# Kernel optimization log

Measured on AMD Instinct MI355X. Metric: run time of the kernel, lower is better.

## Reference

```python
import jax, jax.numpy as jnp
import numpy as np
from itertools import product


def _gen_exps(num_vars, degree):
    return [e for e in product(range(degree + 1), repeat=num_vars) if sum(e) <= degree]

EXPS_W = _gen_exps(4, 3)  # 35 tuples (ex, es, ey, ew)
EXPS_B = _gen_exps(2, 3)  # 10 tuples (ey, eb)


def setup_inputs() -> dict:
    key = jax.random.key(0)
    ks = jax.random.split(key, 7)
    B, D_in, D_out = 8192, 512, 512
    x = jax.random.normal(ks[0], (B, D_in), dtype=jnp.float32)
    s = jax.random.normal(ks[1], (B, D_out), dtype=jnp.float32)
    y = jax.random.normal(ks[2], (B, D_out), dtype=jnp.float32)
    w = jax.random.normal(ks[3], (D_out, D_in), dtype=jnp.float32) * 0.05
    b = jax.random.normal(ks[4], (D_out,), dtype=jnp.float32) * 0.05
    params_w = jax.random.normal(ks[5], (len(EXPS_W),), dtype=jnp.float32) * 0.1
    params_b = jax.random.normal(ks[6], (len(EXPS_B),), dtype=jnp.float32) * 0.1
    return {"x": x, "s": s, "y": y, "w": w, "b": b, "params_w": params_w, "params_b": params_b}


def _dw(x, s, y, w, params_w):
    # unique exponent powers (computed once, reused across the 35 terms)
    px = {e: x ** e for e in {t[0] for t in EXPS_W}}
    ps = {e: s ** e for e in {t[1] for t in EXPS_W}}
    py = {e: y ** e for e in {t[2] for t in EXPS_W}}
    pw = {e: w ** e for e in {t[3] for t in EXPS_W}}
    inv_B = 1.0 / x.shape[0]
    delta_w = jnp.zeros_like(w)
    for i, (ex, es, ey, ew) in enumerate(EXPS_W):
        # (y^ey * s^es).T @ x^ex  -> [out, in]
        corr = jnp.einsum("bo,bi->oi", py[ey] * ps[es], px[ex])
        delta_w = delta_w + (params_w[i] * inv_B) * corr * pw[ew]
    # bound=None -> identity; l2_reg=0.0
    return delta_w


def _db(y, b, params_b):
    py = {e: y ** e for e in {t[0] for t in EXPS_B}}
    pb = {e: b ** e for e in {t[1] for t in EXPS_B}}
    inv_B = 1.0 / y.shape[0]
    delta_b = jnp.zeros_like(b)
    for i, (ey, eb) in enumerate(EXPS_B):
        delta_b = delta_b + (params_b[i] * inv_B) * jnp.sum(py[ey], axis=0) * pb[eb]
    return delta_b


def reference(x, s, y, w, b, params_w, params_b):
    delta_w = _dw(x, s, y, w, params_w)
    delta_b = _db(y, b, params_b)
    return delta_w, delta_b
```

## Files before the change

kernel.cpp:

```cpp
#include <hip/hip_runtime.h>

#define BD 8192
#define DD 512
#define PLANE (BD * DD)
#define NPLANES 5
#define KSPLIT 32
#define NELEM (DD * DD)

typedef __attribute__((ext_vector_type(4))) float f32x4;
typedef __attribute__((ext_vector_type(8))) short short8;

__device__ __forceinline__ float polyev2(float c0, float c1, float c2, float w, float w2) {
    return c0 + c1 * w + c2 * w2;
}

__device__ __forceinline__ unsigned short f2b(float v) {
    unsigned u = __builtin_bit_cast(unsigned, v);
    u += 0x7FFFu + ((u >> 16) & 1u);
    return (unsigned short)(u >> 16);
}

__device__ __forceinline__ void gload_lds16(const unsigned short* g, unsigned short* l) {
    __builtin_amdgcn_global_load_lds((__attribute__((address_space(1))) const void*)g,
                                     (__attribute__((address_space(3))) void*)l, 16, 0, 0);
}


__global__ __launch_bounds__(256, 3) void prep3_kernel(
    const float* __restrict__ x, const float* __restrict__ s,
    const float* __restrict__ y, const float* __restrict__ pw,
    unsigned short* __restrict__ pl, float* __restrict__ csp)
{
    __shared__ char L[5 * 8192];

    const int t      = threadIdx.x;
    const int colL4  = (t & 15) * 4;
    const int rg     = t >> 4;
    const int kl     = rg * 4;
    const int c0     = blockIdx.x * 64;
    const int bt     = blockIdx.y;
    const int r0     = bt * 64;

    const float p23 = pw[23], p24 = pw[24], p25 = pw[25], p26 = pw[26], p27 = pw[27];
    const float p28 = pw[28], p29 = pw[29], p32 = pw[32], p33 = pw[33];

    float sm[12][4];
#pragma unroll
    for (int v = 0; v < 12; ++v)
#pragma unroll
        for (int cc = 0; cc < 4; ++cc) sm[v][cc] = 0.f;

    unsigned pk[NPLANES][4][2];

#pragma unroll
    for (int j = 0; j < 4; ++j) {
        const int row = r0 + kl + j;
        const float4 xv = *(const float4*)&x[(size_t)row * DD + c0 + colL4];
        const float4 sv = *(const float4*)&s[(size_t)row * DD + c0 + colL4];
        const float4 yv = *(const float4*)&y[(size_t)row * DD + c0 + colL4];
        const float xa[4] = {xv.x, xv.y, xv.z, xv.w};
        const float sa[4] = {sv.x, sv.y, sv.z, sv.w};
        const float ya[4] = {yv.x, yv.y, yv.z, yv.w};
#pragma unroll
        for (int cc = 0; cc < 4; ++cc) {
            const float X = xa[cc], S = sa[cc], Y = ya[cc];
            const float X2 = X * X, S2 = S * S, Y2 = Y * Y, SY = S * Y;
            sm[0][cc] += X;  sm[1][cc] += X2;      sm[2][cc] += X2 * X;
            sm[3][cc] += S;  sm[4][cc] += S2;      sm[5][cc] += S2 * S;
            sm[6][cc] += Y;  sm[7][cc] += Y2;      sm[8][cc] += Y2 * Y;
            sm[9][cc] += SY; sm[10][cc] += S2 * Y; sm[11][cc] += S * Y2;
            unsigned short tv[NPLANES];
            tv[0] = f2b(p26 * S + p23 * Y + p29 * S2 + p25 * Y2 + p28 * SY);
            tv[1] = f2b(p33 * S + p32 * Y);
            tv[2] = f2b(p27 * S + p24 * Y);
            tv[3] = f2b(X);
            tv[4] = f2b(X2);
            if ((j & 1) == 0) {
#pragma unroll
                for (int p = 0; p < NPLANES; ++p) pk[p][cc][j >> 1] = (unsigned)tv[p];
            } else {
#pragma unroll
                for (int p = 0; p < NPLANES; ++p) pk[p][cc][j >> 1] |= (unsigned)tv[p] << 16;
            }
        }
    }

#pragma unroll
    for (int p = 0; p < NPLANES; ++p) {
#pragma unroll
        for (int cc = 0; cc < 4; ++cc) {
            const int colL = colL4 + cc;
            const int addr = p * 8192 + colL * 128 + (((kl >> 3) ^ (colL & 7)) << 4) + ((kl & 4) << 1);
            uint2 u; u.x = pk[p][cc][0]; u.y = pk[p][cc][1];
            *(uint2*)&L[addr] = u;
        }
    }
    __syncthreads();

    {
        char* gbase = (char*)pl;
        const size_t blockByte = ((size_t)bt * DD + c0) * 128;
#pragma unroll
        for (int u = 0; u < 10; ++u) {
            const int byteoff = u * 4096 + t * 16;
            const int p = byteoff >> 13;
            const int within = byteoff & 8191;
            *(uint4*)(gbase + ((size_t)p * PLANE) * 2 + blockByte + within) =
                *(const uint4*)&L[byteoff];
        }
    }
    __syncthreads();

#pragma unroll
    for (int v = 0; v < 12; ++v)
#pragma unroll
        for (int cc = 0; cc < 4; ++cc) {
            sm[v][cc] += __shfl_xor(sm[v][cc], 16, 64);
            sm[v][cc] += __shfl_xor(sm[v][cc], 32, 64);
        }
    float* R = (float*)L;
    const int wv = t >> 6, ln = t & 63;
    if (ln < 16) {
#pragma unroll
        for (int v = 0; v < 12; ++v)
#pragma unroll
            for (int cc = 0; cc < 4; ++cc)
                R[(wv * 16 + ln) * 48 + v * 4 + cc] = sm[v][cc];
    }
    __syncthreads();
    if (t < 16) {
        const int blk = bt * 8 + blockIdx.x;
#pragma unroll
        for (int v = 0; v < 12; ++v)
#pragma unroll
            for (int cc = 0; cc < 4; ++cc) {
                float a = R[(0 * 16 + t) * 48 + v * 4 + cc]
                        + R[(1 * 16 + t) * 48 + v * 4 + cc]
                        + R[(2 * 16 + t) * 48 + v * 4 + cc]
                        + R[(3 * 16 + t) * 48 + v * 4 + cc];
                csp[((size_t)blk * 12 + v) * 64 + t * 4 + cc] = a;
            }
    }
}

__global__ __launch_bounds__(256) void reduce_cs_kernel(
    const float* __restrict__ csp, float* __restrict__ cs)
{
    const int u = blockIdx.x * 256 + threadIdx.x;
    if (u < 12 * DD) {
        const int v = u >> 9;
        const int c = u & 511;
        const int colq = c >> 6, cl = c & 63;
        float acc = 0.f;
        for (int bt = 0; bt < 128; ++bt)
            acc += csp[((size_t)(bt * 8 + colq) * 12 + v) * 64 + cl];
        cs[v * DD + c] = acc;
    }
}

__device__ __forceinline__ void do_tile(
    const unsigned short* __restrict__ A, const unsigned short* __restrict__ B,
    int wo, int wi, int l15, int g4, f32x4 (&acc)[4][4])
{
#pragma unroll
    for (int ss = 0; ss < 2; ++ss) {
        short8 af[4], bf[4];
#pragma unroll
        for (int m = 0; m < 4; ++m) {
            const int r = wo + m * 16 + l15;
            af[m] = *(const short8*)((const char*)A + (r << 7) + ((((ss << 2) + g4) ^ (r & 7)) << 4));
        }
#pragma unroll
        for (int n = 0; n < 4; ++n) {
            const int r = wi + n * 16 + l15;
            bf[n] = *(const short8*)((const char*)B + (r << 7) + ((((ss << 2) + g4) ^ (r & 7)) << 4));
        }
#pragma unroll
        for (int m = 0; m < 4; ++m)
#pragma unroll
            for (int n = 0; n < 4; ++n)
                acc[m][n] = __builtin_amdgcn_mfma_f32_16x16x32_bf16(af[m], bf[n], acc[m][n], 0, 0, 0);
    }
}

__global__ __launch_bounds__(256, 2) void gemm_kernel(
    const unsigned short* __restrict__ pl, const float* __restrict__ w,
    float* __restrict__ part)
{
    __shared__ unsigned short lds[2][2][8192];

    const int t    = threadIdx.x;
    const int lane = t & 63;
    const int wid  = t >> 6;
    const int bid  = blockIdx.x;
    const int ks   = (bid & 7) + ((bid >> 7) << 3);
    const int tile = (bid >> 3) & 15;
    const int tileI = tile & 3;
    const int tileO = tile >> 2;
    const int wo = (wid >> 1) * 64, wi = (wid & 1) * 64;
    const int l15 = lane & 15, g4 = lane >> 4;

    const unsigned short* Am = pl + (size_t)(ks < 16 ? 0 : 1) * PLANE;
    const unsigned short* Bm = pl + (size_t)(ks < 16 ? 3 : 4) * PLANE;
    const unsigned short* Aw = pl + (size_t)2 * PLANE;
    const unsigned short* Bx = pl + (size_t)3 * PLANE;
    const int btm0 = (ks & 15) * 8;
    const int btw0 = ks * 4;

    f32x4 accM[4][4], accW[4][4];
#pragma unroll
    for (int m = 0; m < 4; ++m)
#pragma unroll
        for (int n = 0; n < 4; ++n) { accM[m][n] = (f32x4)0.f; accW[m][n] = (f32x4)0.f; }

    auto Abase = [&](int j) -> const unsigned short* {
        return (j < 8) ? Am + ((size_t)(btm0 + j) * DD + tileO * 128) * 64
                       : Aw + ((size_t)(btw0 + j - 8) * DD + tileO * 128) * 64;
    };
    auto Bbase = [&](int j) -> const unsigned short* {
        return (j < 8) ? Bm + ((size_t)(btm0 + j) * DD + tileI * 128) * 64
                       : Bx + ((size_t)(btw0 + j - 8) * DD + tileI * 128) * 64;
    };
    auto stage = [&](const unsigned short* Ag, const unsigned short* Bg, int buf) {
        unsigned short* La = &lds[buf][0][0];
        unsigned short* Lb = &lds[buf][1][0];
#pragma unroll
        for (int c = 0; c < 4; ++c) {
            gload_lds16(Ag + c * 2048 + t * 8, La + c * 2048 + wid * 512);
            gload_lds16(Bg + c * 2048 + t * 8, Lb + c * 2048 + wid * 512);
        }
    };

    stage(Abase(0), Bbase(0), 0);
    __syncthreads();
#pragma unroll 1
    for (int j = 0; j < 8; ++j) {
        const int cur = j & 1;
        stage(Abase(j + 1), Bbase(j + 1), cur ^ 1);
        do_tile(&lds[cur][0][0], &lds[cur][1][0], wo, wi, l15, g4, accM);
        __syncthreads();
    }
#pragma unroll 1
    for (int j = 8; j < 12; ++j) {
        const int cur = j & 1;
        if (j < 11) stage(Abase(j + 1), Bbase(j + 1), cur ^ 1);
        do_tile(&lds[cur][0][0], &lds[cur][1][0], wo, wi, l15, g4, accW);
        __syncthreads();
    }

    float* pout = part + (size_t)ks * NELEM;
#pragma unroll
    for (int m = 0; m < 4; ++m) {
        const int o = tileO * 128 + wo + m * 16 + g4 * 4;
#pragma unroll
        for (int n = 0; n < 4; ++n) {
            const int i = tileI * 128 + wi + n * 16 + l15;
#pragma unroll
            for (int r = 0; r < 4; ++r) {
                const float wv = w[(size_t)(o + r) * DD + i];
                pout[(size_t)(o + r) * DD + i] = accM[m][n][r] + wv * accW[m][n][r];
            }
        }
    }
}

__global__ __launch_bounds__(256) void reduce_rank1_kernel(
    const float* __restrict__ part, const float* __restrict__ w,
    const float* __restrict__ pw, const float* __restrict__ cs,
    float* __restrict__ out)
{
    const int idx = blockIdx.x * 256 + threadIdx.x;
    const int o = idx >> 9;
    const int i = idx & 511;
    float g = 0.f;
#pragma unroll
    for (int ks = 0; ks < KSPLIT; ++ks) g += part[(size_t)ks * NELEM + idx];
    const float wv = w[idx];
    const float w2 = wv * wv, w3 = w2 * wv;
    float acc = (float)BD * (pw[0] + pw[1] * wv + pw[2] * w2 + pw[3] * w3);
    acc += cs[0 * DD + i] * polyev2(pw[20], pw[21], pw[22], wv, w2);
    acc += cs[1 * DD + i] * (pw[30] + pw[31] * wv);
    acc += cs[2 * DD + i] * pw[34];
    acc += cs[6 * DD + o]  * polyev2(pw[4],  pw[5],  pw[6],  wv, w2);
    acc += cs[7 * DD + o]  * (pw[7] + pw[8] * wv);
    acc += cs[8 * DD + o]  * pw[9];
    acc += cs[3 * DD + o]  * polyev2(pw[10], pw[11], pw[12], wv, w2);
    acc += cs[9 * DD + o]  * (pw[13] + pw[14] * wv);
    acc += cs[11 * DD + o] * pw[15];
    acc += cs[4 * DD + o]  * (pw[16] + pw[17] * wv);
    acc += cs[10 * DD + o] * pw[18];
    acc += cs[5 * DD + o]  * pw[19];
    out[idx] = (1.0f / (float)BD) * (g + acc);
}

__global__ __launch_bounds__(256) void deltab_kernel(
    const float* __restrict__ bvec, const float* __restrict__ pb,
    const float* __restrict__ cs, float* __restrict__ out)
{
    const int o = blockIdx.x * 256 + threadIdx.x;
    if (o < DD) {
        const float bv = bvec[o];
        const float b2 = bv * bv, b3 = b2 * bv;
        const float invB = 1.0f / (float)BD;
        float acc = (float)BD * (pb[0] + pb[1] * bv + pb[2] * b2 + pb[3] * b3);
        acc += cs[6 * DD + o] * (pb[4] + pb[5] * bv + pb[6] * b2);
        acc += cs[7 * DD + o] * (pb[7] + pb[8] * bv);
        acc += cs[8 * DD + o] * pb[9];
        out[DD * DD + o] = invB * acc;
    }
}

__global__ __launch_bounds__(256) void prep_old_kernel(
    const float* __restrict__ x, const float* __restrict__ s,
    const float* __restrict__ y, const float* __restrict__ pw,
    unsigned short* __restrict__ pl, float* __restrict__ cs)
{
    const int t  = threadIdx.x;
    const int o  = blockIdx.x * 64 + (t & 63);
    const int bt = blockIdx.y * 4 + (t >> 6);
    const int b0 = bt * 32;
    const float p23 = pw[23], p24 = pw[24], p25 = pw[25], p26 = pw[26], p27 = pw[27];
    const float p28 = pw[28], p29 = pw[29], p32 = pw[32], p33 = pw[33];
    float xs1 = 0.f, xs2 = 0.f, xs3 = 0.f;
    float ss1 = 0.f, ss2 = 0.f, ss3 = 0.f;
    float ys1 = 0.f, ys2 = 0.f, ys3 = 0.f;
    float sy1 = 0.f, s2y = 0.f, sy2 = 0.f;
    unsigned pk[NPLANES][16];
#pragma unroll
    for (int j = 0; j < 32; ++j) {
        const size_t off = (size_t)(b0 + j) * DD + o;
        const float xv = x[off], sv = s[off], yv = y[off];
        const float xq = xv * xv, sq = sv * sv, yq = yv * yv, syv = sv * yv;
        xs1 += xv;  xs2 += xq;      xs3 += xq * xv;
        ss1 += sv;  ss2 += sq;      ss3 += sq * sv;
        ys1 += yv;  ys2 += yq;      ys3 += yq * yv;
        sy1 += syv; s2y += sq * yv; sy2 += sv * yq;
        unsigned short tmp[NPLANES];
        tmp[0] = f2b(p26 * sv + p23 * yv + p29 * sq + p25 * yq + p28 * syv);
        tmp[1] = f2b(p33 * sv + p32 * yv);
        tmp[2] = f2b(p27 * sv + p24 * yv);
        tmp[3] = f2b(xv);
        tmp[4] = f2b(xq);
        if ((j & 1) == 0) {
#pragma unroll
            for (int p = 0; p < NPLANES; ++p) pk[p][j >> 1] = (unsigned)tmp[p];
        } else {
#pragma unroll
            for (int p = 0; p < NPLANES; ++p) pk[p][j >> 1] |= (unsigned)tmp[p] << 16;
        }
    }
    const size_t wbase = ((size_t)bt * DD + o) * 32;
#pragma unroll
    for (int p = 0; p < NPLANES; ++p) {
        uint4* dst = (uint4*)(pl + (size_t)p * PLANE + wbase);
#pragma unroll
        for (int c = 0; c < 4; ++c) {
            uint4 u;
            u.x = pk[p][c * 4 + 0]; u.y = pk[p][c * 4 + 1];
            u.z = pk[p][c * 4 + 2]; u.w = pk[p][c * 4 + 3];
            dst[c] = u;
        }
    }
    atomicAdd(&cs[0 * DD + o], xs1);  atomicAdd(&cs[1 * DD + o], xs2);  atomicAdd(&cs[2 * DD + o], xs3);
    atomicAdd(&cs[3 * DD + o], ss1);  atomicAdd(&cs[4 * DD + o], ss2);  atomicAdd(&cs[5 * DD + o], ss3);
    atomicAdd(&cs[6 * DD + o], ys1);  atomicAdd(&cs[7 * DD + o], ys2);  atomicAdd(&cs[8 * DD + o], ys3);
    atomicAdd(&cs[9 * DD + o], sy1);  atomicAdd(&cs[10 * DD + o], s2y); atomicAdd(&cs[11 * DD + o], sy2);
}

__global__ __launch_bounds__(256) void gemm3_kernel(
    const unsigned short* __restrict__ pl, const float* __restrict__ w,
    float* __restrict__ out)
{
    __shared__ unsigned short ldsA[128 * 32];
    __shared__ unsigned short ldsB[128 * 32];
    const int t    = threadIdx.x;
    const int lane = t & 63;
    const int wid  = t >> 6;
    const int g     = blockIdx.z;
    const int tileI = blockIdx.x & 3;
    const int tileO = blockIdx.x >> 2;
    const int kt0   = blockIdx.y * 16;
    const int aplane = (g == 0) ? 0 : (g == 1) ? 1 : 2;
    const int bplane = (g == 1) ? 4 : 3;
    const unsigned short* Ap = pl + (size_t)aplane * PLANE;
    const unsigned short* Bp = pl + (size_t)bplane * PLANE;
    const int wo = (wid >> 1) * 64;
    const int wi = (wid & 1) * 64;
    const int l15 = lane & 15;
    const int kchunk = (lane >> 4) * 8;
    f32x4 acc[4][4];
#pragma unroll
    for (int m = 0; m < 4; ++m)
#pragma unroll
        for (int n = 0; n < 4; ++n) acc[m][n] = (f32x4)0.f;
    unsigned short* ldsAw = ldsA + wid * 512;
    unsigned short* ldsBw = ldsB + wid * 512;
    const size_t tg = (size_t)t * 8;
    for (int kt = 0; kt < 16; ++kt) {
        const size_t abase = ((size_t)(kt0 + kt) * DD + tileO * 128) * 32;
        const size_t bbase = ((size_t)(kt0 + kt) * DD + tileI * 128) * 32;
        __syncthreads();
        gload_lds16(Ap + abase + tg,        ldsAw);
        gload_lds16(Ap + abase + 2048 + tg, ldsAw + 2048);
        gload_lds16(Bp + bbase + tg,        ldsBw);
        gload_lds16(Bp + bbase + 2048 + tg, ldsBw + 2048);
        __syncthreads();
        short8 af[4], bf[4];
#pragma unroll
        for (int m = 0; m < 4; ++m)
            af[m] = *(const short8*)&ldsA[(wo + m * 16 + l15) * 32 + kchunk];
#pragma unroll
        for (int n = 0; n < 4; ++n)
            bf[n] = *(const short8*)&ldsB[(wi + n * 16 + l15) * 32 + kchunk];
#pragma unroll
        for (int m = 0; m < 4; ++m)
#pragma unroll
            for (int n = 0; n < 4; ++n)
                acc[m][n] = __builtin_amdgcn_mfma_f32_16x16x32_bf16(af[m], bf[n], acc[m][n], 0, 0, 0);
    }
    const float invB = 1.0f / (float)BD;
    const int l4 = lane >> 4;
#pragma unroll
    for (int m = 0; m < 4; ++m) {
#pragma unroll
        for (int n = 0; n < 4; ++n) {
#pragma unroll
            for (int r = 0; r < 4; ++r) {
                const int o = tileO * 128 + wo + m * 16 + l4 * 4 + r;
                const int i = tileI * 128 + wi + n * 16 + l15;
                float v = acc[m][n][r] * invB;
                if (g == 2) v *= w[o * DD + i];
                atomicAdd(&out[o * DD + i], v);
            }
        }
    }
}

__global__ __launch_bounds__(256) void rank1_kernel(
    const float* __restrict__ w, const float* __restrict__ pw,
    const float* __restrict__ cs, float* __restrict__ out)
{
    const int idx = blockIdx.x * 256 + threadIdx.x;
    const int o = idx >> 9;
    const int i = idx & 511;
    const float wv = w[idx];
    const float w2 = wv * wv, w3 = w2 * wv;
    const float invB = 1.0f / (float)BD;
    float acc = (float)BD * (pw[0] + pw[1] * wv + pw[2] * w2 + pw[3] * w3);
    acc += cs[0 * DD + i] * polyev2(pw[20], pw[21], pw[22], wv, w2);
    acc += cs[1 * DD + i] * (pw[30] + pw[31] * wv);
    acc += cs[2 * DD + i] * pw[34];
    acc += cs[6 * DD + o]  * polyev2(pw[4],  pw[5],  pw[6],  wv, w2);
    acc += cs[7 * DD + o]  * (pw[7] + pw[8] * wv);
    acc += cs[8 * DD + o]  * pw[9];
    acc += cs[3 * DD + o]  * polyev2(pw[10], pw[11], pw[12], wv, w2);
    acc += cs[9 * DD + o]  * (pw[13] + pw[14] * wv);
    acc += cs[11 * DD + o] * pw[15];
    acc += cs[4 * DD + o]  * (pw[16] + pw[17] * wv);
    acc += cs[10 * DD + o] * pw[18];
    acc += cs[5 * DD + o]  * pw[19];
    out[idx] += invB * acc;
}

extern "C" void kernel_launch(void* const* d_in, const int* in_sizes, int n_in,
                              void* d_out, int out_size, void* d_ws, size_t ws_size,
                              hipStream_t stream) {
    const float* x  = (const float*)d_in[0];
    const float* s  = (const float*)d_in[1];
    const float* y  = (const float*)d_in[2];
    const float* w  = (const float*)d_in[3];
    const float* b  = (const float*)d_in[4];
    const float* pw = (const float*)d_in[5];
    const float* pb = (const float*)d_in[6];
    float* out = (float*)d_out;

    const size_t planeBytes = (size_t)PLANE * 2 * NPLANES;
    const size_t partBytes  = (size_t)KSPLIT * NELEM * sizeof(float);
    const size_t cspBytes   = (size_t)1024 * 12 * 64 * sizeof(float);
    const size_t csBytes    = 12 * DD * sizeof(float);

    if (ws_size >= planeBytes + partBytes + cspBytes + csBytes) {
        unsigned short* pl = (unsigned short*)d_ws;
        float* part = (float*)((char*)d_ws + planeBytes);
        float* csp  = (float*)((char*)d_ws + planeBytes + partBytes);
        float* cs   = (float*)((char*)d_ws + planeBytes + partBytes + cspBytes);
        prep3_kernel<<<dim3(8, 128), 256, 0, stream>>>(x, s, y, pw, pl, csp);
        reduce_cs_kernel<<<24, 256, 0, stream>>>(csp, cs);
        gemm_kernel<<<512, 256, 0, stream>>>(pl, w, part);
        reduce_rank1_kernel<<<1024, 256, 0, stream>>>(part, w, pw, cs, out);
        deltab_kernel<<<2, 256, 0, stream>>>(b, pb, cs, out);
    } else {
        unsigned short* pl = (unsigned short*)d_ws;
        float* cs = (float*)((char*)d_ws + planeBytes);
        hipMemsetAsync(cs, 0, csBytes, stream);
        hipMemsetAsync(out, 0, (size_t)out_size * sizeof(float), stream);
        prep_old_kernel<<<dim3(8, 64), 256, 0, stream>>>(x, s, y, pw, pl, cs);
        gemm3_kernel<<<dim3(16, 16, 3), 256, 0, stream>>>(pl, w, out);
        rank1_kernel<<<dim3((DD * DD) / 256), 256, 0, stream>>>(w, pw, cs, out);
        deltab_kernel<<<2, 256, 0, stream>>>(b, pb, cs, out);
    }
}
```

Measured before the change: 138.1 us.

## Fuse all stages into one cooperative persistent kernel with grid syncs

```diff
diff --git a/kernel.cpp b/kernel.cpp
--- a/kernel.cpp
+++ b/kernel.cpp
@@ -1,4 +1,7 @@
 #include <hip/hip_runtime.h>
+#include <hip/hip_cooperative_groups.h>
+
+namespace cg = cooperative_groups;
 
 #define BD 8192
 #define DD 512
@@ -26,19 +29,17 @@
 }
 
 
-__global__ __launch_bounds__(256, 3) void prep3_kernel(
+__device__ __forceinline__ void prep_unit(
     const float* __restrict__ x, const float* __restrict__ s,
     const float* __restrict__ y, const float* __restrict__ pw,
-    unsigned short* __restrict__ pl, float* __restrict__ csp)
-{
-    __shared__ char L[5 * 8192];
-
+    unsigned short* __restrict__ pl, float* __restrict__ csp,
+    const int colq, const int bt, char* L)
+{
     const int t      = threadIdx.x;
     const int colL4  = (t & 15) * 4;
     const int rg     = t >> 4;
     const int kl     = rg * 4;
-    const int c0     = blockIdx.x * 64;
-    const int bt     = blockIdx.y;
+    const int c0     = colq * 64;
     const int r0     = bt * 64;
 
     const float p23 = pw[23], p24 = pw[24], p25 = pw[25], p26 = pw[26], p27 = pw[27];
@@ -85,6 +86,8 @@
         }
     }
 
+    __syncthreads();
+
 #pragma unroll
     for (int p = 0; p < NPLANES; ++p) {
 #pragma unroll
@@ -129,7 +132,7 @@
     }
     __syncthreads();
     if (t < 16) {
-        const int blk = bt * 8 + blockIdx.x;
+        const int blk = bt * 8 + colq;
 #pragma unroll
         for (int v = 0; v < 12; ++v)
 #pragma unroll
@@ -143,21 +146,6 @@
     }
 }
 
-__global__ __launch_bounds__(256) void reduce_cs_kernel(
-    const float* __restrict__ csp, float* __restrict__ cs)
-{
-    const int u = blockIdx.x * 256 + threadIdx.x;
-    if (u < 12 * DD) {
-        const int v = u >> 9;
-        const int c = u & 511;
-        const int colq = c >> 6, cl = c & 63;
-        float acc = 0.f;
-        for (int bt = 0; bt < 128; ++bt)
-            acc += csp[((size_t)(bt * 8 + colq) * 12 + v) * 64 + cl];
-        cs[v * DD + c] = acc;
-    }
-}
-
 __device__ __forceinline__ void do_tile(
     const unsigned short* __restrict__ A, const unsigned short* __restrict__ B,
     int wo, int wi, int l15, int g4, f32x4 (&acc)[4][4])
@@ -183,16 +171,13 @@
     }
 }
 
-__global__ __launch_bounds__(256, 2) void gemm_kernel(
+__device__ __forceinline__ void gemm_body(
     const unsigned short* __restrict__ pl, const float* __restrict__ w,
-    float* __restrict__ part)
-{
-    __shared__ unsigned short lds[2][2][8192];
-
+    float* __restrict__ part, const int bid, unsigned short* ldsp)
+{
     const int t    = threadIdx.x;
     const int lane = t & 63;
     const int wid  = t >> 6;
-    const int bid  = blockIdx.x;
     const int ks   = (bid & 7) + ((bid >> 7) << 3);
     const int tile = (bid >> 3) & 15;
     const int tileI = tile & 3;
@@ -222,8 +207,8 @@
                        : Bx + ((size_t)(btw0 + j - 8) * DD + tileI * 128) * 64;
     };
     auto stage = [&](const unsigned short* Ag, const unsigned short* Bg, int buf) {
-        unsigned short* La = &lds[buf][0][0];
-        unsigned short* Lb = &lds[buf][1][0];
+        unsigned short* La = ldsp + (buf * 2 + 0) * 8192;
+        unsigned short* Lb = ldsp + (buf * 2 + 1) * 8192;
 #pragma unroll
         for (int c = 0; c < 4; ++c) {
             gload_lds16(Ag + c * 2048 + t * 8, La + c * 2048 + wid * 512);
@@ -237,14 +222,14 @@
     for (int j = 0; j < 8; ++j) {
         const int cur = j & 1;
         stage(Abase(j + 1), Bbase(j + 1), cur ^ 1);
-        do_tile(&lds[cur][0][0], &lds[cur][1][0], wo, wi, l15, g4, accM);
+        do_tile(ldsp + (cur * 2 + 0) * 8192, ldsp + (cur * 2 + 1) * 8192, wo, wi, l15, g4, accM);
         __syncthreads();
     }
 #pragma unroll 1
     for (int j = 8; j < 12; ++j) {
         const int cur = j & 1;
         if (j < 11) stage(Abase(j + 1), Bbase(j + 1), cur ^ 1);
-        do_tile(&lds[cur][0][0], &lds[cur][1][0], wo, wi, l15, g4, accW);
+        do_tile(ldsp + (cur * 2 + 0) * 8192, ldsp + (cur * 2 + 1) * 8192, wo, wi, l15, g4, accW);
         __syncthreads();
     }
 
@@ -264,12 +249,10 @@
     }
 }
 
-__global__ __launch_bounds__(256) void reduce_rank1_kernel(
-    const float* __restrict__ part, const float* __restrict__ w,
-    const float* __restrict__ pw, const float* __restrict__ cs,
-    float* __restrict__ out)
-{
-    const int idx = blockIdx.x * 256 + threadIdx.x;
+__device__ __forceinline__ void rank1_store(
+    const int idx, const float* __restrict__ part, const float* __restrict__ w,
+    const float* __restrict__ pw, const float* __restrict__ cs, float* __restrict__ out)
+{
     const int o = idx >> 9;
     const int i = idx & 511;
     float g = 0.f;
@@ -293,173 +276,125 @@
     out[idx] = (1.0f / (float)BD) * (g + acc);
 }
 
+__device__ __forceinline__ void deltab_store(
+    const int o, const float* __restrict__ bvec, const float* __restrict__ pb,
+    const float* __restrict__ cs, float* __restrict__ out)
+{
+    const float bv = bvec[o];
+    const float b2 = bv * bv, b3 = b2 * bv;
+    const float invB = 1.0f / (float)BD;
+    float acc = (float)BD * (pb[0] + pb[1] * bv + pb[2] * b2 + pb[3] * b3);
+    acc += cs[6 * DD + o] * (pb[4] + pb[5] * bv + pb[6] * b2);
+    acc += cs[7 * DD + o] * (pb[7] + pb[8] * bv);
+    acc += cs[8 * DD + o] * pb[9];
+    out[DD * DD + o] = invB * acc;
+}
+
+__global__ __launch_bounds__(256, 2) void fused_all(
+    const float* __restrict__ x, const float* __restrict__ s,
+    const float* __restrict__ y, const float* __restrict__ w,
+    const float* __restrict__ bvec, const float* __restrict__ pw,
+    const float* __restrict__ pb,
+    unsigned short* __restrict__ pl, float* __restrict__ part,
+    float* __restrict__ csp, float* __restrict__ cs, float* __restrict__ out)
+{
+    __shared__ __align__(16) char L[65536];
+    const int bid = blockIdx.x;
+    const int t   = threadIdx.x;
+    cg::grid_group grid = cg::this_grid();
+
+    prep_unit(x, s, y, pw, pl, csp, (2 * bid) & 7,     (2 * bid) >> 3,     L);
+    prep_unit(x, s, y, pw, pl, csp, (2 * bid + 1) & 7, (2 * bid + 1) >> 3, L);
+
+    __threadfence();
+    grid.sync();
+
+    {
+        float* red = (float*)L;
+        if (t < 192) {
+            const int e = t >> 4, j = t & 15;
+            const int u = bid * 12 + e;
+            const int v = u >> 9, c = u & 511;
+            const int cq = c >> 6, cl = c & 63;
+            float p = 0.f;
+#pragma unroll
+            for (int k = 0; k < 8; ++k) {
+                const int bt = j * 8 + k;
+                p += csp[((size_t)(bt * 8 + cq) * 12 + v) * 64 + cl];
+            }
+            red[e * 16 + j] = p;
+        }
+        __syncthreads();
+        if (t < 12) {
+            float a = 0.f;
+#pragma unroll
+            for (int j2 = 0; j2 < 16; ++j2) a += red[t * 16 + j2];
+            const int u = bid * 12 + t;
+            cs[(u >> 9) * DD + (u & 511)] = a;
+        }
+        __syncthreads();
+    }
+
+    gemm_body(pl, w, part, bid, (unsigned short*)L);
+
+    __threadfence();
+    grid.sync();
+
+    const int base = bid * 256 + t;
+    rank1_store(base,          part, w, pw, cs, out);
+    rank1_store(base + 131072, part, w, pw, cs, out);
+    if (bid == 0) {
+        deltab_store(t,       bvec, pb, cs, out);
+        deltab_store(t + 256, bvec, pb, cs, out);
+    }
+}
+
+__global__ __launch_bounds__(256, 3) void prep3_kernel(
+    const float* __restrict__ x, const float* __restrict__ s,
+    const float* __restrict__ y, const float* __restrict__ pw,
+    unsigned short* __restrict__ pl, float* __restrict__ csp)
+{
+    __shared__ __align__(16) char L[5 * 8192];
+    prep_unit(x, s, y, pw, pl, csp, blockIdx.x, blockIdx.y, L);
+}
+
+__global__ __launch_bounds__(256) void reduce_cs_kernel(
+    const float* __restrict__ csp, float* __restrict__ cs)
+{
+    const int u = blockIdx.x * 256 + threadIdx.x;
+    if (u < 12 * DD) {
+        const int v = u >> 9;
+        const int c = u & 511;
+        const int colq = c >> 6, cl = c & 63;
+        float acc = 0.f;
+        for (int bt = 0; bt < 128; ++bt)
+            acc += csp[((size_t)(bt * 8 + colq) * 12 + v) * 64 + cl];
+        cs[v * DD + c] = acc;
+    }
+}
+
+__global__ __launch_bounds__(256, 2) void gemm_kernel(
+    const unsigned short* __restrict__ pl, const float* __restrict__ w,
+    float* __restrict__ part)
+{
+    __shared__ unsigned short lds[4][8192];
+    gemm_body(pl, w, part, blockIdx.x, &lds[0][0]);
+}
+
+__global__ __launch_bounds__(256) void reduce_rank1_kernel(
+    const float* __restrict__ part, const float* __restrict__ w,
+    const float* __restrict__ pw, const float* __restrict__ cs,
+    float* __restrict__ out)
+{
+    rank1_store(blockIdx.x * 256 + threadIdx.x, part, w, pw, cs, out);
+}
+
 __global__ __launch_bounds__(256) void deltab_kernel(
     const float* __restrict__ bvec, const float* __restrict__ pb,
     const float* __restrict__ cs, float* __restrict__ out)
 {
     const int o = blockIdx.x * 256 + threadIdx.x;
-    if (o < DD) {
-        const float bv = bvec[o];
-        const float b2 = bv * bv, b3 = b2 * bv;
-        const float invB = 1.0f / (float)BD;
-        float acc = (float)BD * (pb[0] + pb[1] * bv + pb[2] * b2 + pb[3] * b3);
-        acc += cs[6 * DD + o] * (pb[4] + pb[5] * bv + pb[6] * b2);
-        acc += cs[7 * DD + o] * (pb[7] + pb[8] * bv);
-        acc += cs[8 * DD + o] * pb[9];
-        out[DD * DD + o] = invB * acc;
-    }
-}
-
-__global__ __launch_bounds__(256) void prep_old_kernel(
-    const float* __restrict__ x, const float* __restrict__ s,
-    const float* __restrict__ y, const float* __restrict__ pw,
-    unsigned short* __restrict__ pl, float* __restrict__ cs)
-{
-    const int t  = threadIdx.x;
-    const int o  = blockIdx.x * 64 + (t & 63);
-    const int bt = blockIdx.y * 4 + (t >> 6);
-    const int b0 = bt * 32;
-    const float p23 = pw[23], p24 = pw[24], p25 = pw[25], p26 = pw[26], p27 = pw[27];
-    const float p28 = pw[28], p29 = pw[29], p32 = pw[32], p33 = pw[33];
-    float xs1 = 0.f, xs2 = 0.f, xs3 = 0.f;
-    float ss1 = 0.f, ss2 = 0.f, ss3 = 0.f;
-    float ys1 = 0.f, ys2 = 0.f, ys3 = 0.f;
-    float sy1 = 0.f, s2y = 0.f, sy2 = 0.f;
-    unsigned pk[NPLANES][16];
-#pragma unroll
-    for (int j = 0; j < 32; ++j) {
-        const size_t off = (size_t)(b0 + j) * DD + o;
-        const float xv = x[off], sv = s[off], yv = y[off];
-        const float xq = xv * xv, sq = sv * sv, yq = yv * yv, syv = sv * yv;
-        xs1 += xv;  xs2 += xq;      xs3 += xq * xv;
-        ss1 += sv;  ss2 += sq;      ss3 += sq * sv;
-        ys1 += yv;  ys2 += yq;      ys3 += yq * yv;
-        sy1 += syv; s2y += sq * yv; sy2 += sv * yq;
-        unsigned short tmp[NPLANES];
-        tmp[0] = f2b(p26 * sv + p23 * yv + p29 * sq + p25 * yq + p28 * syv);
-        tmp[1] = f2b(p33 * sv + p32 * yv);
-        tmp[2] = f2b(p27 * sv + p24 * yv);
-        tmp[3] = f2b(xv);
-        tmp[4] = f2b(xq);
-        if ((j & 1) == 0) {
-#pragma unroll
-            for (int p = 0; p < NPLANES; ++p) pk[p][j >> 1] = (unsigned)tmp[p];
-        } else {
-#pragma unroll
-            for (int p = 0; p < NPLANES; ++p) pk[p][j >> 1] |= (unsigned)tmp[p] << 16;
-        }
-    }
-    const size_t wbase = ((size_t)bt * DD + o) * 32;
-#pragma unroll
-    for (int p = 0; p < NPLANES; ++p) {
-        uint4* dst = (uint4*)(pl + (size_t)p * PLANE + wbase);
-#pragma unroll
-        for (int c = 0; c < 4; ++c) {
-            uint4 u;
-            u.x = pk[p][c * 4 + 0]; u.y = pk[p][c * 4 + 1];
-            u.z = pk[p][c * 4 + 2]; u.w = pk[p][c * 4 + 3];
-            dst[c] = u;
-        }
-    }
-    atomicAdd(&cs[0 * DD + o], xs1);  atomicAdd(&cs[1 * DD + o], xs2);  atomicAdd(&cs[2 * DD + o], xs3);
-    atomicAdd(&cs[3 * DD + o], ss1);  atomicAdd(&cs[4 * DD + o], ss2);  atomicAdd(&cs[5 * DD + o], ss3);
-    atomicAdd(&cs[6 * DD + o], ys1);  atomicAdd(&cs[7 * DD + o], ys2);  atomicAdd(&cs[8 * DD + o], ys3);
-    atomicAdd(&cs[9 * DD + o], sy1);  atomicAdd(&cs[10 * DD + o], s2y); atomicAdd(&cs[11 * DD + o], sy2);
-}
-
-__global__ __launch_bounds__(256) void gemm3_kernel(
-    const unsigned short* __restrict__ pl, const float* __restrict__ w,
-    float* __restrict__ out)
-{
-    __shared__ unsigned short ldsA[128 * 32];
-    __shared__ unsigned short ldsB[128 * 32];
-    const int t    = threadIdx.x;
-    const int lane = t & 63;
-    const int wid  = t >> 6;
-    const int g     = blockIdx.z;
-    const int tileI = blockIdx.x & 3;
-    const int tileO = blockIdx.x >> 2;
-    const int kt0   = blockIdx.y * 16;
-    const int aplane = (g == 0) ? 0 : (g == 1) ? 1 : 2;
-    const int bplane = (g == 1) ? 4 : 3;
-    const unsigned short* Ap = pl + (size_t)aplane * PLANE;
-    const unsigned short* Bp = pl + (size_t)bplane * PLANE;
-    const int wo = (wid >> 1) * 64;
-    const int wi = (wid & 1) * 64;
-    const int l15 = lane & 15;
-    const int kchunk = (lane >> 4) * 8;
-    f32x4 acc[4][4];
-#pragma unroll
-    for (int m = 0; m < 4; ++m)
-#pragma unroll
-        for (int n = 0; n < 4; ++n) acc[m][n] = (f32x4)0.f;
-    unsigned short* ldsAw = ldsA + wid * 512;
-    unsigned short* ldsBw = ldsB + wid * 512;
-    const size_t tg = (size_t)t * 8;
-    for (int kt = 0; kt < 16; ++kt) {
-        const size_t abase = ((size_t)(kt0 + kt) * DD + tileO * 128) * 32;
-        const size_t bbase = ((size_t)(kt0 + kt) * DD + tileI * 128) * 32;
-        __syncthreads();
-        gload_lds16(Ap + abase + tg,        ldsAw);
-        gload_lds16(Ap + abase + 2048 + tg, ldsAw + 2048);
-        gload_lds16(Bp + bbase + tg,        ldsBw);
-        gload_lds16(Bp + bbase + 2048 + tg, ldsBw + 2048);
-        __syncthreads();
-        short8 af[4], bf[4];
-#pragma unroll
-        for (int m = 0; m < 4; ++m)
-            af[m] = *(const short8*)&ldsA[(wo + m * 16 + l15) * 32 + kchunk];
-#pragma unroll
-        for (int n = 0; n < 4; ++n)
-            bf[n] = *(const short8*)&ldsB[(wi + n * 16 + l15) * 32 + kchunk];
-#pragma unroll
-        for (int m = 0; m < 4; ++m)
-#pragma unroll
-            for (int n = 0; n < 4; ++n)
-                acc[m][n] = __builtin_amdgcn_mfma_f32_16x16x32_bf16(af[m], bf[n], acc[m][n], 0, 0, 0);
-    }
-    const float invB = 1.0f / (float)BD;
-    const int l4 = lane >> 4;
-#pragma unroll
-    for (int m = 0; m < 4; ++m) {
-#pragma unroll
-        for (int n = 0; n < 4; ++n) {
-#pragma unroll
-            for (int r = 0; r < 4; ++r) {
-                const int o = tileO * 128 + wo + m * 16 + l4 * 4 + r;
-                const int i = tileI * 128 + wi + n * 16 + l15;
-                float v = acc[m][n][r] * invB;
-                if (g == 2) v *= w[o * DD + i];
-                atomicAdd(&out[o * DD + i], v);
-            }
-        }
-    }
-}
-
-__global__ __launch_bounds__(256) void rank1_kernel(
-    const float* __restrict__ w, const float* __restrict__ pw,
-    const float* __restrict__ cs, float* __restrict__ out)
-{
-    const int idx = blockIdx.x * 256 + threadIdx.x;
-    const int o = idx >> 9;
-    const int i = idx & 511;
-    const float wv = w[idx];
-    const float w2 = wv * wv, w3 = w2 * wv;
-    const float invB = 1.0f / (float)BD;
-    float acc = (float)BD * (pw[0] + pw[1] * wv + pw[2] * w2 + pw[3] * w3);
-    acc += cs[0 * DD + i] * polyev2(pw[20], pw[21], pw[22], wv, w2);
-    acc += cs[1 * DD + i] * (pw[30] + pw[31] * wv);
-    acc += cs[2 * DD + i] * pw[34];
-    acc += cs[6 * DD + o]  * polyev2(pw[4],  pw[5],  pw[6],  wv, w2);
-    acc += cs[7 * DD + o]  * (pw[7] + pw[8] * wv);
-    acc += cs[8 * DD + o]  * pw[9];
-    acc += cs[3 * DD + o]  * polyev2(pw[10], pw[11], pw[12], wv, w2);
-    acc += cs[9 * DD + o]  * (pw[13] + pw[14] * wv);
-    acc += cs[11 * DD + o] * pw[15];
-    acc += cs[4 * DD + o]  * (pw[16] + pw[17] * wv);
-    acc += cs[10 * DD + o] * pw[18];
-    acc += cs[5 * DD + o]  * pw[19];
-    out[idx] += invB * acc;
+    if (o < DD) deltab_store(o, bvec, pb, cs, out);
 }
 
 extern "C" void kernel_launch(void* const* d_in, const int* in_sizes, int n_in,
@@ -477,26 +412,24 @@
     const size_t planeBytes = (size_t)PLANE * 2 * NPLANES;
     const size_t partBytes  = (size_t)KSPLIT * NELEM * sizeof(float);
     const size_t cspBytes   = (size_t)1024 * 12 * 64 * sizeof(float);
-    const size_t csBytes    = 12 * DD * sizeof(float);
-
-    if (ws_size >= planeBytes + partBytes + cspBytes + csBytes) {
-        unsigned short* pl = (unsigned short*)d_ws;
-        float* part = (float*)((char*)d_ws + planeBytes);
-        float* csp  = (float*)((char*)d_ws + planeBytes + partBytes);
-        float* cs   = (float*)((char*)d_ws + planeBytes + partBytes + cspBytes);
+
+    unsigned short* pl = (unsigned short*)d_ws;
+    float* part = (float*)((char*)d_ws + planeBytes);
+    float* csp  = (float*)((char*)d_ws + planeBytes + partBytes);
+    float* cs   = (float*)((char*)d_ws + planeBytes + partBytes + cspBytes);
+
+    void* args[] = { (void*)&x, (void*)&s, (void*)&y, (void*)&w, (void*)&b,
+                     (void*)&pw, (void*)&pb, (void*)&pl, (void*)&part,
+                     (void*)&csp, (void*)&cs, (void*)&out };
+    hipError_t err = hipLaunchCooperativeKernel(
+        (const void*)fused_all, dim3(512), dim3(256), args, 0, stream);
+
+    if (err != hipSuccess) {
+        (void)hipGetLastError();
         prep3_kernel<<<dim3(8, 128), 256, 0, stream>>>(x, s, y, pw, pl, csp);
         reduce_cs_kernel<<<24, 256, 0, stream>>>(csp, cs);
         gemm_kernel<<<512, 256, 0, stream>>>(pl, w, part);
         reduce_rank1_kernel<<<1024, 256, 0, stream>>>(part, w, pw, cs, out);
         deltab_kernel<<<2, 256, 0, stream>>>(b, pb, cs, out);
-    } else {
-        unsigned short* pl = (unsigned short*)d_ws;
-        float* cs = (float*)((char*)d_ws + planeBytes);
-        hipMemsetAsync(cs, 0, csBytes, stream);
-        hipMemsetAsync(out, 0, (size_t)out_size * sizeof(float), stream);
-        prep_old_kernel<<<dim3(8, 64), 256, 0, stream>>>(x, s, y, pw, pl, cs);
-        gemm3_kernel<<<dim3(16, 16, 3), 256, 0, stream>>>(pl, w, out);
-        rank1_kernel<<<dim3((DD * DD) / 256), 256, 0, stream>>>(w, pw, cs, out);
-        deltab_kernel<<<2, 256, 0, stream>>>(b, pb, cs, out);
-    }
-}
+    }
+}
```

After: 391.8 us. 2.84x slower.
